# Kernel tuning notes

Hardware: AMD Instinct MI355X
Metric: run time of the kernel (lower is better)

The kernel has to match this reference:

```python
import jax, jax.numpy as jnp
import numpy as np

N, IN_F, OUT_F = 8192, 512, 256
ALPHA = 0.2  # leaky_relu negative slope
NEG_INF = -1e18


def setup_inputs() -> dict:
    key = jax.random.key(0)
    k1, k2, k3, k4 = jax.random.split(key, 4)
    h = jax.random.normal(k1, (N, IN_F), dtype=jnp.float32)
    adj = jax.random.randint(k2, (N, N), 0, 2, dtype=jnp.int32)
    # W: Linear(in_features, out_features, bias=False); stored [in, out] for x @ W
    lim_w = float(np.sqrt(6.0 / (IN_F + OUT_F)))
    W = jax.random.uniform(k3, (IN_F, OUT_F), minval=-lim_w, maxval=lim_w, dtype=jnp.float32)
    # a_T: Linear(2*out_features, 1); split into a1 (for H1=Wh_i) and a2 (for H2=Wh_j)
    lim_a = float(np.sqrt(6.0 / (2 * OUT_F + 1)))
    a = jax.random.uniform(k4, (2 * OUT_F,), minval=-lim_a, maxval=lim_a, dtype=jnp.float32)
    a1, a2 = a[:OUT_F], a[OUT_F:]
    return {"h": h, "adj": adj, "W": W, "a1": a1, "a2": a2}


def reference(h, adj, W, a1, a2):
    Wh = h @ W  # [N, F]
    # e_ij = leaky_relu(a . [Wh_i, Wh_j]) = leaky_relu(Wh_i.a1 + Wh_j.a2)
    # (mathematically identical to repeat+cat+linear, without the [N,N,2F] tensor)
    src = Wh @ a1  # [N]
    dst = Wh @ a2  # [N]
    e = jax.nn.leaky_relu(src[:, None] + dst[None, :], negative_slope=ALPHA)  # [N, N]
    masked_e = jnp.where(adj > 0, e, jnp.float32(NEG_INF))
    attn = jax.nn.softmax(masked_e, axis=-1)  # [N, N]
    h_prime = attn @ Wh  # [N, F]
    return jax.nn.elu(h_prime)
```

## Files before the change

### kernel.cpp

```cpp
#include <hip/hip_runtime.h>
#include <hip/hip_bf16.h>

#define NN 8192
#define KIN 512
#define KOUT 256
#define ALPHA 0.2f
#define BK 64
#define ROWS 128
#define KQ (NN / 4)
#define NT4 (KQ / BK)

typedef __bf16 bf16x8 __attribute__((ext_vector_type(8)));
typedef float f32x4 __attribute__((ext_vector_type(4)));
typedef unsigned short ushort8_t __attribute__((ext_vector_type(8)));
typedef unsigned short ushort4_t __attribute__((ext_vector_type(4)));
typedef int int4v __attribute__((ext_vector_type(4)));

__device__ __forceinline__ float lrelu(float x) { return x > 0.f ? x : ALPHA * x; }

__device__ __forceinline__ unsigned short f2bf(float f) {
  union { float f; unsigned u; } v; v.f = f;
  unsigned r = v.u + 0x7fffu + ((v.u >> 16) & 1u);
  return (unsigned short)(r >> 16);
}
__device__ __forceinline__ float bf2f(unsigned short b) {
  union { unsigned u; float f; } v; v.u = ((unsigned)b) << 16;
  return v.f;
}

__global__ __launch_bounds__(512) void k_wh(const float* __restrict__ h,
                                            const float* __restrict__ W,
                                            const float* __restrict__ a1,
                                            const float* __restrict__ a2,
                                            unsigned short* __restrict__ WhB,
                                            float* __restrict__ src,
                                            float* __restrict__ dstv) {
  __shared__ float sA[16][36];
  __shared__ float sB[16][260];
  const int tid = threadIdx.x;
  const int wave = tid >> 6;
  const int lane = tid & 63;
  const int bm = blockIdx.x * 32;
  const int arow = tid >> 4;
  const int akk = tid & 15;
  const int bkr = tid >> 5;
  const int bc = (tid & 31) * 8;
  float acc[4][4] = {};
  for (int k0 = 0; k0 < KIN; k0 += 16) {
    float av = h[(size_t)(bm + arow) * KIN + k0 + akk];
    const float4* wp = (const float4*)(W + (size_t)(k0 + bkr) * KOUT + bc);
    float4 w0 = wp[0], w1 = wp[1];
    __syncthreads();
    sA[akk][arow] = av;
    *(float4*)&sB[bkr][bc] = w0;
    *(float4*)&sB[bkr][bc + 4] = w1;
    __syncthreads();
#pragma unroll
    for (int k = 0; k < 16; ++k) {
      float4 a4 = *(const float4*)&sA[k][wave * 4];
      float4 b4 = *(const float4*)&sB[k][lane * 4];
      float aa[4] = {a4.x, a4.y, a4.z, a4.w};
      float bb[4] = {b4.x, b4.y, b4.z, b4.w};
#pragma unroll
      for (int i = 0; i < 4; ++i)
#pragma unroll
        for (int jj = 0; jj < 4; ++jj)
          acc[i][jj] = fmaf(aa[i], bb[jj], acc[i][jj]);
    }
  }
  float4 a1v = *(const float4*)(a1 + lane * 4);
  float4 a2v = *(const float4*)(a2 + lane * 4);
  float sp[4], dp[4];
#pragma unroll
  for (int i = 0; i < 4; ++i) {
    sp[i] = acc[i][0] * a1v.x + acc[i][1] * a1v.y + acc[i][2] * a1v.z + acc[i][3] * a1v.w;
    dp[i] = acc[i][0] * a2v.x + acc[i][1] * a2v.y + acc[i][2] * a2v.z + acc[i][3] * a2v.w;
  }
#pragma unroll
  for (int off = 32; off >= 1; off >>= 1) {
#pragma unroll
    for (int i = 0; i < 4; ++i) {
      sp[i] += __shfl_xor(sp[i], off);
      dp[i] += __shfl_xor(dp[i], off);
    }
  }
  if (lane == 0) {
#pragma unroll
    for (int i = 0; i < 4; ++i) {
      src[bm + wave * 4 + i] = sp[i];
      dstv[bm + wave * 4 + i] = dp[i];
    }
  }
#pragma unroll
  for (int i = 0; i < 4; ++i) {
    ushort4_t pk;
#pragma unroll
    for (int jj = 0; jj < 4; ++jj) pk[jj] = f2bf(acc[i][jj]);
    *(ushort4_t*)(WhB + (size_t)(bm + wave * 4 + i) * KOUT + lane * 4) = pk;
  }
}

__global__ __launch_bounds__(256) void k_trF(const unsigned short* __restrict__ WhB,
                                             unsigned short* __restrict__ WhF) {
  __shared__ unsigned int sX[64][65];
  const int t = threadIdx.x;
  const int r0 = (blockIdx.x & 127) * 64;
  const int c0 = (blockIdx.x >> 7) * 64;
  const int rr = t >> 2;
  const int cq = (t & 3) * 16;
  const ushort8_t* p = (const ushort8_t*)(WhB + (size_t)(r0 + rr) * KOUT + c0 + cq);
  ushort8_t v0 = p[0], v1 = p[1];
#pragma unroll
  for (int i = 0; i < 8; ++i) {
    sX[rr][cq + i] = v0[i];
    sX[rr][cq + 8 + i] = v1[i];
  }
  __syncthreads();
  const int wv = t >> 6;
  const int lane = t & 63;
  const int q = lane >> 4;
  const int fr = lane & 15;
  const int kt = r0 >> 6;
  const int wbase = c0 >> 5;
#pragma unroll
  for (int i = 0; i < 2; ++i) {
    const int g = wv * 2 + i;
    const int wloc = g >> 2;
    const int nc = (g >> 1) & 1;
    const int kh = g & 1;
    const int j0 = kh * 32 + q * 8;
    const int lc = wloc * 32 + nc * 16 + fr;
    ushort8_t o;
#pragma unroll
    for (int e = 0; e < 8; ++e) o[e] = (unsigned short)sX[j0 + e][lc];
    const int w = wbase + wloc;
    const size_t idx = ((((size_t)kt * 8 + w) * 2 + nc) * 2 + kh) * 64 + lane;
    *(ushort8_t*)(WhF + idx * 8) = o;
  }
}

__global__ __launch_bounds__(256) void k_dmax(const float* __restrict__ dstv,
                                              float* __restrict__ Dp) {
  __shared__ float red[256];
  const int t = threadIdx.x;
  float m = -3e38f;
  for (int i = t; i < NN; i += 256) m = fmaxf(m, dstv[i]);
  red[t] = m;
  __syncthreads();
  for (int s = 128; s >= 1; s >>= 1) {
    if (t < s) red[t] = fmaxf(red[t], red[t + s]);
    __syncthreads();
  }
  if (t == 0) *Dp = red[0];
}

struct Bset { ushort8_t b[2][2]; };

#define MF(a, b, c) __builtin_amdgcn_mfma_f32_16x16x32_bf16(a, b, c, 0, 0, 0)

#define BAR()                                              \
  {                                                        \
    asm volatile("s_waitcnt lgkmcnt(0)" ::: "memory");     \
    __builtin_amdgcn_s_barrier();                          \
    asm volatile("" ::: "memory");                         \
  }

#define TI(t) (((t) + ph0) & (NT4 - 1))

#define LOADB(BS, ktl)                                                 \
  {                                                                    \
    const unsigned short* p_ = bfw + (size_t)(ktl) * 16384;            \
    BS.b[0][0] = *(const ushort8_t*)(p_);                              \
    BS.b[0][1] = *(const ushort8_t*)(p_ + 512);                        \
    BS.b[1][0] = *(const ushort8_t*)(p_ + 1024);                       \
    BS.b[1][1] = *(const ushort8_t*)(p_ + 1536);                       \
  }

#define WGEN4(AJ, ktl, koff, buf)                                      \
  {                                                                    \
    float4 dv = *(const float4*)&sD[(ktl) * BK + (koff)];              \
    float w0 = (AJ.x > 0) ? __expf(lrelu(s_r + dv.x) - c_r) : 0.f;     \
    float w1 = (AJ.y > 0) ? __expf(lrelu(s_r + dv.y) - c_r) : 0.f;     \
    float w2 = (AJ.z > 0) ? __expf(lrelu(s_r + dv.z) - c_r) : 0.f;     \
    float w3 = (AJ.w > 0) ? __expf(lrelu(s_r + dv.w) - c_r) : 0.f;     \
    unsigned short u0 = f2bf(w0), u1 = f2bf(w1);                       \
    unsigned short u2 = f2bf(w2), u3 = f2bf(w3);                       \
    lsum += bf2f(u0) + bf2f(u1) + bf2f(u2) + bf2f(u3);                 \
    uint2 pk;                                                          \
    pk.x = (unsigned)u0 | ((unsigned)u1 << 16);                        \
    pk.y = (unsigned)u2 | ((unsigned)u3 << 16);                        \
    *(uint2*)(sAb + (buf) * 16384 +                                    \
              ((pr * 128 + (koff) * 2) ^ ((pr & 7) << 4))) = pk;       \
  }

#define WGEN16(A0, A1, A2, A3, ktl, buf)                               \
  {                                                                    \
    WGEN4(A0, ktl, pk16 + 0, buf);                                     \
    WGEN4(A1, ktl, pk16 + 4, buf);                                     \
    WGEN4(A2, ktl, pk16 + 8, buf);                                     \
    WGEN4(A3, ktl, pk16 + 12, buf);                                    \
  }

#define LOADADJ16(A0, A1, A2, A3, ktl)                                 \
  {                                                                    \
    const int4v* ap = (const int4v*)(adjp + (size_t)(ktl) * BK);       \
    A0 = __builtin_nontemporal_load(ap);                               \
    A1 = __builtin_nontemporal_load(ap + 1);                           \
    A2 = __builtin_nontemporal_load(ap + 2);                           \
    A3 = __builtin_nontemporal_load(ap + 3);                           \
  }

#define LDA(cur, mr, kk)                                                        \
  __builtin_bit_cast(bf16x8,                                                    \
    *(const ushort8_t*)(sAb + (cur) * 16384 +                                   \
      ((((mr) * 16 + fr) * 128 + (kk) * 64 + fq * 16) ^ ((fr & 7) << 4))))

#define MSTEP(cur, BS)                                                 \
  {                                                                    \
    _Pragma("unroll")                                                  \
    for (int mr = 0; mr < 8; ++mr) {                                   \
      bf16x8 a0 = LDA(cur, mr, 0), a1 = LDA(cur, mr, 1);               \
      acc[mr][0] = MF(a0, BS.b[0][0], acc[mr][0]);                     \
      acc[mr][0] = MF(a1, BS.b[0][1], acc[mr][0]);                     \
      acc[mr][1] = MF(a0, BS.b[1][0], acc[mr][1]);                     \
      acc[mr][1] = MF(a1, BS.b[1][1], acc[mr][1]);                     \
    }                                                                  \
  }

__global__ __launch_bounds__(1024) void k_attn(const int* __restrict__ adj,
                                               const unsigned short* __restrict__ WhF,
                                               const float* __restrict__ src,
                                               const float* __restrict__ dstv,
                                               const float* __restrict__ Dp,
                                               float* __restrict__ Pbuf,
                                               float* __restrict__ Lsum) {
  __shared__ unsigned short sA[2][ROWS][BK];
  __shared__ float sD[KQ];
  char* sAb = (char*)&sA[0][0][0];
  const int tid = threadIdx.x;
  const int lane = tid & 63;
  const int wave = tid >> 6;
  const int qtr = blockIdx.x & 3;
  const int rg = blockIdx.x >> 2;
  const int r0 = rg * ROWS;
  const int ph0 = rg & (NT4 - 1);
  const int kbase = qtr * KQ;
  const float D = *Dp;

  *(float2*)&sD[tid * 2] = *(const float2*)(dstv + kbase + tid * 2);
  __syncthreads();

  const int ptid = tid - 512;
  const int pr = ptid >> 2;
  const int pk16 = (ptid & 3) * 16;
  const float s_r = src[r0 + pr];
  const float c_r = lrelu(s_r + D);
  const int* adjp = adj + (size_t)(r0 + pr) * NN + kbase + pk16;
  float lsum = 0.f;

  const int fr = lane & 15;
  const int fq = lane >> 4;
  const unsigned short* bfw =
      WhF + ((size_t)(qtr * NT4) * 8 + wave) * 2048 + lane * 8;
  f32x4 acc[8][2];
#pragma unroll
  for (int mr = 0; mr < 8; ++mr) {
    acc[mr][0] = (f32x4){0.f, 0.f, 0.f, 0.f};
    acc[mr][1] = (f32x4){0.f, 0.f, 0.f, 0.f};
  }
  Bset B0, B1;
  int4v aA0, aA1, aA2, aA3;
  int4v aB0, aB1, aB2, aB3;

  if (wave >= 8) {
    int4v d0, d1, d2, d3;
    {
      const int4v* ap = (const int4v*)(adjp + (size_t)TI(0) * BK);
      d0 = ap[0]; d1 = ap[1]; d2 = ap[2]; d3 = ap[3];
    }
    WGEN16(d0, d1, d2, d3, TI(0), 0);
    LOADADJ16(aB0, aB1, aB2, aB3, TI(1));
    LOADADJ16(aA0, aA1, aA2, aA3, TI(2));
  } else {
    LOADB(B0, TI(0));
    LOADB(B1, TI(1));
  }
  BAR();

  if (wave < 8) {
#pragma unroll 1
    for (int p = 0; p < NT4; p += 2) {
      { MSTEP(0, B0); LOADB(B0, TI(p + 2)); BAR(); }
      { MSTEP(1, B1); LOADB(B1, TI(p + 3)); BAR(); }
    }
#pragma unroll
    for (int mr = 0; mr < 8; ++mr) {
#pragma unroll
      for (int r = 0; r < 4; ++r) {
        const int row = mr * 16 + fq * 4 + r;
#pragma unroll
        for (int nc = 0; nc < 2; ++nc) {
          const int col = wave * 32 + nc * 16 + fr;
          Pbuf[(size_t)(qtr * NN + r0 + row) * KOUT + col] = acc[mr][nc][r];
        }
      }
    }
  } else {
#pragma unroll 1
    for (int p = 0; p < NT4; p += 2) {
      {
        WGEN16(aB0, aB1, aB2, aB3, TI(p + 1), 1);
        LOADADJ16(aB0, aB1, aB2, aB3, TI(p + 3));
        BAR();
      }
      {
        if (p + 2 < NT4) { WGEN16(aA0, aA1, aA2, aA3, TI(p + 2), 0); }
        LOADADJ16(aA0, aA1, aA2, aA3, TI(p + 4));
        BAR();
      }
    }
    lsum += __shfl_xor(lsum, 1, 4);
    lsum += __shfl_xor(lsum, 2, 4);
    if ((ptid & 3) == 0) Lsum[qtr * NN + r0 + pr] = lsum;
  }
}

__global__ __launch_bounds__(256) void k_comb(const float* __restrict__ Pbuf,
                                              const float* __restrict__ Lsum,
                                              float* __restrict__ out) {
  const int t = threadIdx.x;
  const int row = blockIdx.x * 4 + (t >> 6);
  const int col = (t & 63) * 4;
  const float l = Lsum[row] + Lsum[NN + row] + Lsum[2 * NN + row] + Lsum[3 * NN + row];
  float4 p0 = *(const float4*)(Pbuf + (size_t)row * KOUT + col);
  float4 p1 = *(const float4*)(Pbuf + (size_t)(NN + row) * KOUT + col);
  float4 p2 = *(const float4*)(Pbuf + (size_t)(2 * NN + row) * KOUT + col);
  float4 p3 = *(const float4*)(Pbuf + (size_t)(3 * NN + row) * KOUT + col);
  float4 v;
  v.x = (p0.x + p1.x + p2.x + p3.x) / l;
  v.y = (p0.y + p1.y + p2.y + p3.y) / l;
  v.z = (p0.z + p1.z + p2.z + p3.z) / l;
  v.w = (p0.w + p1.w + p2.w + p3.w) / l;
  v.x = v.x > 0.f ? v.x : __expf(v.x) - 1.f;
  v.y = v.y > 0.f ? v.y : __expf(v.y) - 1.f;
  v.z = v.z > 0.f ? v.z : __expf(v.z) - 1.f;
  v.w = v.w > 0.f ? v.w : __expf(v.w) - 1.f;
  *(float4*)(out + (size_t)row * KOUT + col) = v;
}

extern "C" void kernel_launch(void* const* d_in, const int* in_sizes, int n_in,
                              void* d_out, int out_size, void* d_ws, size_t ws_size,
                              hipStream_t stream) {
  const float* h = (const float*)d_in[0];
  const int* adj = (const int*)d_in[1];
  const float* W = (const float*)d_in[2];
  const float* a1 = (const float*)d_in[3];
  const float* a2 = (const float*)d_in[4];
  float* out = (float*)d_out;

  unsigned short* WhB = (unsigned short*)d_ws;
  unsigned short* WhF = WhB + (size_t)NN * KOUT;
  float* src = (float*)(WhF + (size_t)NN * KOUT);
  float* dstv = src + NN;
  float* Dp = dstv + NN;
  float* Pbuf = Dp + 16;
  float* Lsum = Pbuf + (size_t)4 * NN * KOUT;

  hipLaunchKernelGGL(k_wh, dim3(NN / 32), dim3(512), 0, stream, h, W, a1, a2, WhB, src, dstv);
  hipLaunchKernelGGL(k_trF, dim3(512), dim3(256), 0, stream, WhB, WhF);
  hipLaunchKernelGGL(k_dmax, dim3(1), dim3(256), 0, stream, dstv, Dp);
  hipLaunchKernelGGL(k_attn, dim3(256), dim3(1024), 0, stream, adj, WhF, src, dstv, Dp, Pbuf, Lsum);
  hipLaunchKernelGGL(k_comb, dim3(NN / 4), dim3(256), 0, stream, Pbuf, Lsum, out);
}
```

Baseline: 149.9 us.

## Retile MFMA waves to 64x64 and stream B halves; use packed bf16 convert

The eight MFMA waves each owned 128 rows by 32 columns. They now use a 2x4 grid, so each wave covers a 64x64 tile. This halves the LDS A-fragment reads per wave per K-step. Global B loads are split into two halves, and the second half plus the next tile's first half are issued in the middle of the MFMA sequence to overlap with compute. The weight generator also switches to v_cvt_pk_bf16_f32, uses fmax for leaky ReLU, and sums the unrounded fp32 weights, which slightly changes normalisation relative to the bf16 values fed to the matmul.

Result: slower. 161.5 us (+7.8%).

```diff
diff --git a/kernel.cpp b/kernel.cpp
--- a/kernel.cpp
+++ b/kernel.cpp
@@ -23,9 +23,11 @@
   unsigned r = v.u + 0x7fffu + ((v.u >> 16) & 1u);
   return (unsigned short)(r >> 16);
 }
-__device__ __forceinline__ float bf2f(unsigned short b) {
-  union { unsigned u; float f; } v; v.u = ((unsigned)b) << 16;
-  return v.f;
+
+__device__ __forceinline__ unsigned cvt_pk_bf16(float lo, float hi) {
+  unsigned r;
+  asm("v_cvt_pk_bf16_f32 %0, %1, %2" : "=v"(r) : "v"(lo), "v"(hi));
+  return r;
 }
 
 __global__ __launch_bounds__(512) void k_wh(const float* __restrict__ h,
@@ -154,7 +156,6 @@
   if (t == 0) *Dp = red[0];
 }
 
-struct Bset { ushort8_t b[2][2]; };
 
 #define MF(a, b, c) __builtin_amdgcn_mfma_f32_16x16x32_bf16(a, b, c, 0, 0, 0)
 
@@ -167,28 +168,28 @@
 
 #define TI(t) (((t) + ph0) & (NT4 - 1))
 
-#define LOADB(BS, ktl)                                                 \
+#define LOADB_H(dst, ktl, hh)                                          \
   {                                                                    \
-    const unsigned short* p_ = bfw + (size_t)(ktl) * 16384;            \
-    BS.b[0][0] = *(const ushort8_t*)(p_);                              \
-    BS.b[0][1] = *(const ushort8_t*)(p_ + 512);                        \
-    BS.b[1][0] = *(const ushort8_t*)(p_ + 1024);                       \
-    BS.b[1][1] = *(const ushort8_t*)(p_ + 1536);                       \
+    const unsigned short* p_ = bfw + (size_t)(ktl) * 16384 + (hh) * 512; \
+    dst[0] = *(const ushort8_t*)(p_);                                  \
+    dst[1] = *(const ushort8_t*)(p_ + 1024);                           \
+    dst[2] = *(const ushort8_t*)(p_ + 2048);                           \
+    dst[3] = *(const ushort8_t*)(p_ + 3072);                           \
   }
 
 #define WGEN4(AJ, ktl, koff, buf)                                      \
   {                                                                    \
     float4 dv = *(const float4*)&sD[(ktl) * BK + (koff)];              \
-    float w0 = (AJ.x > 0) ? __expf(lrelu(s_r + dv.x) - c_r) : 0.f;     \
-    float w1 = (AJ.y > 0) ? __expf(lrelu(s_r + dv.y) - c_r) : 0.f;     \
-    float w2 = (AJ.z > 0) ? __expf(lrelu(s_r + dv.z) - c_r) : 0.f;     \
-    float w3 = (AJ.w > 0) ? __expf(lrelu(s_r + dv.w) - c_r) : 0.f;     \
-    unsigned short u0 = f2bf(w0), u1 = f2bf(w1);                       \
-    unsigned short u2 = f2bf(w2), u3 = f2bf(w3);                       \
-    lsum += bf2f(u0) + bf2f(u1) + bf2f(u2) + bf2f(u3);                 \
+    float x0 = s_r + dv.x, x1 = s_r + dv.y;                            \
+    float x2 = s_r + dv.z, x3 = s_r + dv.w;                            \
+    float w0 = (AJ.x > 0) ? __expf(fmaxf(x0, ALPHA * x0) - c_r) : 0.f; \
+    float w1 = (AJ.y > 0) ? __expf(fmaxf(x1, ALPHA * x1) - c_r) : 0.f; \
+    float w2 = (AJ.z > 0) ? __expf(fmaxf(x2, ALPHA * x2) - c_r) : 0.f; \
+    float w3 = (AJ.w > 0) ? __expf(fmaxf(x3, ALPHA * x3) - c_r) : 0.f; \
+    lsum += (w0 + w1) + (w2 + w3);                                     \
     uint2 pk;                                                          \
-    pk.x = (unsigned)u0 | ((unsigned)u1 << 16);                        \
-    pk.y = (unsigned)u2 | ((unsigned)u3 << 16);                        \
+    pk.x = cvt_pk_bf16(w0, w1);                                        \
+    pk.y = cvt_pk_bf16(w2, w3);                                        \
     *(uint2*)(sAb + (buf) * 16384 +                                    \
               ((pr * 128 + (koff) * 2) ^ ((pr & 7) << 4))) = pk;       \
   }
@@ -213,18 +214,48 @@
 #define LDA(cur, mr, kk)                                                        \
   __builtin_bit_cast(bf16x8,                                                    \
     *(const ushort8_t*)(sAb + (cur) * 16384 +                                   \
-      ((((mr) * 16 + fr) * 128 + (kk) * 64 + fq * 16) ^ ((fr & 7) << 4))))
-
-#define MSTEP(cur, BS)                                                 \
+      (((wr64 + (mr) * 16 + fr) * 128 + (kk) * 64 + fq * 16) ^ ((fr & 7) << 4))))
+
+#define MSTEP(cur, ktl, ktln)                                          \
   {                                                                    \
-    _Pragma("unroll")                                                  \
-    for (int mr = 0; mr < 8; ++mr) {                                   \
-      bf16x8 a0 = LDA(cur, mr, 0), a1 = LDA(cur, mr, 1);               \
-      acc[mr][0] = MF(a0, BS.b[0][0], acc[mr][0]);                     \
-      acc[mr][0] = MF(a1, BS.b[0][1], acc[mr][0]);                     \
-      acc[mr][1] = MF(a0, BS.b[1][0], acc[mr][1]);                     \
-      acc[mr][1] = MF(a1, BS.b[1][1], acc[mr][1]);                     \
-    }                                                                  \
+    bf16x8 a0 = LDA(cur, 0, 0), a1 = LDA(cur, 1, 0);                   \
+    bf16x8 a2 = LDA(cur, 2, 0), a3 = LDA(cur, 3, 0);                   \
+    LOADB_H(Bh1, (ktl), 1);                                            \
+    acc[0][0] = MF(a0, Bh0[0], acc[0][0]);                             \
+    acc[0][1] = MF(a0, Bh0[1], acc[0][1]);                             \
+    acc[0][2] = MF(a0, Bh0[2], acc[0][2]);                             \
+    acc[0][3] = MF(a0, Bh0[3], acc[0][3]);                             \
+    acc[1][0] = MF(a1, Bh0[0], acc[1][0]);                             \
+    acc[1][1] = MF(a1, Bh0[1], acc[1][1]);                             \
+    acc[1][2] = MF(a1, Bh0[2], acc[1][2]);                             \
+    acc[1][3] = MF(a1, Bh0[3], acc[1][3]);                             \
+    acc[2][0] = MF(a2, Bh0[0], acc[2][0]);                             \
+    acc[2][1] = MF(a2, Bh0[1], acc[2][1]);                             \
+    acc[2][2] = MF(a2, Bh0[2], acc[2][2]);                             \
+    acc[2][3] = MF(a2, Bh0[3], acc[2][3]);                             \
+    acc[3][0] = MF(a3, Bh0[0], acc[3][0]);                             \
+    acc[3][1] = MF(a3, Bh0[1], acc[3][1]);                             \
+    acc[3][2] = MF(a3, Bh0[2], acc[3][2]);                             \
+    acc[3][3] = MF(a3, Bh0[3], acc[3][3]);                             \
+    a0 = LDA(cur, 0, 1); a1 = LDA(cur, 1, 1);                          \
+    a2 = LDA(cur, 2, 1); a3 = LDA(cur, 3, 1);                          \
+    LOADB_H(Bh0, (ktln), 0);                                           \
+    acc[0][0] = MF(a0, Bh1[0], acc[0][0]);                             \
+    acc[0][1] = MF(a0, Bh1[1], acc[0][1]);                             \
+    acc[0][2] = MF(a0, Bh1[2], acc[0][2]);                             \
+    acc[0][3] = MF(a0, Bh1[3], acc[0][3]);                             \
+    acc[1][0] = MF(a1, Bh1[0], acc[1][0]);                             \
+    acc[1][1] = MF(a1, Bh1[1], acc[1][1]);                             \
+    acc[1][2] = MF(a1, Bh1[2], acc[1][2]);                             \
+    acc[1][3] = MF(a1, Bh1[3], acc[1][3]);                             \
+    acc[2][0] = MF(a2, Bh1[0], acc[2][0]);                             \
+    acc[2][1] = MF(a2, Bh1[1], acc[2][1]);                             \
+    acc[2][2] = MF(a2, Bh1[2], acc[2][2]);                             \
+    acc[2][3] = MF(a2, Bh1[3], acc[2][3]);                             \
+    acc[3][0] = MF(a3, Bh1[0], acc[3][0]);                             \
+    acc[3][1] = MF(a3, Bh1[1], acc[3][1]);                             \
+    acc[3][2] = MF(a3, Bh1[2], acc[3][2]);                             \
+    acc[3][3] = MF(a3, Bh1[3], acc[3][3]);                             \
   }
 
 __global__ __launch_bounds__(1024) void k_attn(const int* __restrict__ adj,
@@ -260,15 +291,16 @@
 
   const int fr = lane & 15;
   const int fq = lane >> 4;
+  const int wr64 = (wave >> 2) * 64;
+  const int wc = wave & 3;
   const unsigned short* bfw =
-      WhF + ((size_t)(qtr * NT4) * 8 + wave) * 2048 + lane * 8;
-  f32x4 acc[8][2];
-#pragma unroll
-  for (int mr = 0; mr < 8; ++mr) {
-    acc[mr][0] = (f32x4){0.f, 0.f, 0.f, 0.f};
-    acc[mr][1] = (f32x4){0.f, 0.f, 0.f, 0.f};
-  }
-  Bset B0, B1;
+      WhF + ((size_t)(qtr * NT4) * 8 + wc * 2) * 2048 + lane * 8;
+  f32x4 acc[4][4];
+#pragma unroll
+  for (int mr = 0; mr < 4; ++mr)
+#pragma unroll
+    for (int nc = 0; nc < 4; ++nc) acc[mr][nc] = (f32x4){0.f, 0.f, 0.f, 0.f};
+  ushort8_t Bh0[4], Bh1[4];
   int4v aA0, aA1, aA2, aA3;
   int4v aB0, aB1, aB2, aB3;
 
@@ -282,25 +314,29 @@
     LOADADJ16(aB0, aB1, aB2, aB3, TI(1));
     LOADADJ16(aA0, aA1, aA2, aA3, TI(2));
   } else {
-    LOADB(B0, TI(0));
-    LOADB(B1, TI(1));
+    LOADB_H(Bh0, TI(0), 0);
   }
   BAR();
 
   if (wave < 8) {
 #pragma unroll 1
     for (int p = 0; p < NT4; p += 2) {
-      { MSTEP(0, B0); LOADB(B0, TI(p + 2)); BAR(); }
-      { MSTEP(1, B1); LOADB(B1, TI(p + 3)); BAR(); }
-    }
-#pragma unroll
-    for (int mr = 0; mr < 8; ++mr) {
+      MSTEP(0, TI(p), TI(p + 1));
+      BAR();
+      {
+        const int tn = (p + 2 < NT4) ? p + 2 : NT4 - 1;
+        MSTEP(1, TI(p + 1), TI(tn));
+      }
+      BAR();
+    }
+#pragma unroll
+    for (int mr = 0; mr < 4; ++mr) {
 #pragma unroll
       for (int r = 0; r < 4; ++r) {
-        const int row = mr * 16 + fq * 4 + r;
-#pragma unroll
-        for (int nc = 0; nc < 2; ++nc) {
-          const int col = wave * 32 + nc * 16 + fr;
+        const int row = wr64 + mr * 16 + fq * 4 + r;
+#pragma unroll
+        for (int nc = 0; nc < 4; ++nc) {
+          const int col = wc * 64 + nc * 16 + fr;
           Pbuf[(size_t)(qtr * NN + r0 + row) * KOUT + col] = acc[mr][nc][r];
         }
       }
```
